# Performance work log

Measured on AMD Instinct MI355X. Metric: run time of the kernel, lower is better.

The kernel has to match this reference:

```python
import jax, jax.numpy as jnp
import numpy as np

N_NODES = 100000
N_EDGES = 600000
F_IN, F_HID, F_OUT = 128, 256, 24
EPS = 0.0  # GINConv default eps=0, train_eps=False


def setup_inputs() -> dict:
    key = jax.random.key(0)
    k1, k2, k3, k4, k5 = jax.random.split(key, 5)
    features = jax.random.normal(k1, (N_NODES, F_IN), dtype=jnp.float32)
    edge_index = jax.random.randint(k2, (2, N_EDGES), 0, N_NODES, dtype=jnp.int64)
    W1 = jax.random.normal(k3, (F_IN, F_HID), dtype=jnp.float32) * (1.0 / np.sqrt(F_IN))
    b1 = jnp.zeros((F_HID,), dtype=jnp.float32)
    W2 = jax.random.normal(k4, (F_HID, F_OUT), dtype=jnp.float32) * (1.0 / np.sqrt(F_HID))
    b2 = jnp.zeros((F_OUT,), dtype=jnp.float32)
    return {"features": features, "edge_index": edge_index,
            "W1": W1, "b1": b1, "W2": W2, "b2": b2}


def gin_conv(x, src, dst, W, b):
    # sum-aggregate neighbor features: agg[i] = sum_{(j->i)} x[j]
    agg = jax.ops.segment_sum(x[src], dst, num_segments=N_NODES)
    h = (1.0 + EPS) * x + agg
    return h @ W + b


def reference(features, edge_index, W1, b1, W2, b2):
    src, dst = edge_index[0], edge_index[1]
    h = gin_conv(features, src, dst, W1, b1)
    h = jax.nn.relu(h)
    # dropout is identity in eval mode (training=False)
    h = gin_conv(h, src, dst, W2, b2)
    return jax.nn.log_softmax(h, axis=1)
```

## Files before the change

### kernel.cpp

```cpp
#include <hip/hip_runtime.h>
#include <hip/hip_bf16.h>
#include <math.h>

#define N_NODES 100000
#define N_EDGES 600000
#define F_IN 128
#define F_HID 256
#define F_OUT 24
#define SCAN_NB 98

typedef __attribute__((ext_vector_type(8))) short bf16x8;
typedef __attribute__((ext_vector_type(4))) float f32x4;

__device__ inline unsigned short f2bf(float f) {
  __hip_bfloat16 h = __float2bfloat16(f);
  return *reinterpret_cast<unsigned short*>(&h);
}
__device__ inline float bf2f(unsigned short u) {
  return __uint_as_float(((unsigned int)u) << 16);
}

__global__ __launch_bounds__(256) void hist_rank(const int* __restrict__ dst,
                                                 int* __restrict__ deg,
                                                 int* __restrict__ rank) {
  int e = blockIdx.x * 256 + threadIdx.x;
  if (e >= N_EDGES) return;
  rank[e] = atomicAdd(&deg[dst[e]], 1);
}

__global__ __launch_bounds__(256) void scan_partial(
    const int* __restrict__ deg, int* __restrict__ blocksum) {
  int t = threadIdx.x;
  int base = blockIdx.x * 1024 + t * 4;
  int s = 0;
  if (base + 3 < N_NODES) {
    int4 v = *(const int4*)(deg + base);
    s = v.x + v.y + v.z + v.w;
  } else {
    for (int i = base; i < N_NODES; ++i) s += deg[i];
  }
  __shared__ int red[4];
#pragma unroll
  for (int off = 32; off >= 1; off >>= 1) s += __shfl_down(s, off, 64);
  if ((t & 63) == 0) red[t >> 6] = s;
  __syncthreads();
  if (t == 0) blocksum[blockIdx.x] = red[0] + red[1] + red[2] + red[3];
}

__global__ __launch_bounds__(128) void scan_blocksums(int* __restrict__ bs) {
  __shared__ int sh[128];
  int t = threadIdx.x;
  int v = (t < SCAN_NB) ? bs[t] : 0;
  sh[t] = v;
  __syncthreads();
  for (int off = 1; off < 128; off <<= 1) {
    int u = (t >= off) ? sh[t - off] : 0;
    __syncthreads();
    sh[t] += u;
    __syncthreads();
  }
  if (t < SCAN_NB) bs[t] = sh[t] - v;
}

__global__ __launch_bounds__(256) void scan_final(
    const int* __restrict__ deg, const int* __restrict__ blocksum,
    int* __restrict__ row_start) {
  __shared__ int sh[256];
  int t = threadIdx.x;
  int base = blockIdx.x * 1024 + t * 4;
  int d[4] = {0, 0, 0, 0};
  if (base + 3 < N_NODES) {
    int4 v = *(const int4*)(deg + base);
    d[0] = v.x; d[1] = v.y; d[2] = v.z; d[3] = v.w;
  } else {
#pragma unroll
    for (int i = 0; i < 4; ++i)
      if (base + i < N_NODES) d[i] = deg[base + i];
  }
  int ts = d[0] + d[1] + d[2] + d[3];
  sh[t] = ts;
  __syncthreads();
  for (int off = 1; off < 256; off <<= 1) {
    int u = (t >= off) ? sh[t - off] : 0;
    __syncthreads();
    sh[t] += u;
    __syncthreads();
  }
  int run = blocksum[blockIdx.x] + sh[t] - ts;
#pragma unroll
  for (int i = 0; i < 4; ++i) {
    if (base + i < N_NODES) row_start[base + i] = run;
    run += d[i];
  }
}

__global__ __launch_bounds__(256) void fill_csr(
    const int* __restrict__ src, const int* __restrict__ dst,
    const int* __restrict__ row_start, const int* __restrict__ rank,
    int* __restrict__ eidx) {
  int e = blockIdx.x * 256 + threadIdx.x;
  if (e >= N_EDGES) return;
  eidx[row_start[dst[e]] + rank[e]] = src[e];
}

__global__ __launch_bounds__(256) void prep_xbf(
    const float* __restrict__ x, unsigned int* __restrict__ xb) {
  const int n8 = N_NODES * F_IN / 8;
  int i = blockIdx.x * 256 + threadIdx.x;
  int stride = gridDim.x * 256;
  for (; i < n8; i += stride) {
    float4 a = ((const float4*)x)[i * 2];
    float4 b = ((const float4*)x)[i * 2 + 1];
    uint4 o;
    o.x = (unsigned)f2bf(a.x) | ((unsigned)f2bf(a.y) << 16);
    o.y = (unsigned)f2bf(a.z) | ((unsigned)f2bf(a.w) << 16);
    o.z = (unsigned)f2bf(b.x) | ((unsigned)f2bf(b.y) << 16);
    o.w = (unsigned)f2bf(b.z) | ((unsigned)f2bf(b.w) << 16);
    ((uint4*)xb)[i] = o;
  }
}

__global__ __launch_bounds__(256) void prep_w1t(
    const float* __restrict__ W1, unsigned short* __restrict__ w1t) {
  int i = blockIdx.x * 256 + threadIdx.x;
  if (i >= F_IN * F_HID) return;
  int n = i >> 7, k = i & 127;
  w1t[i] = f2bf(W1[k * F_HID + n]);
}

__global__ __launch_bounds__(256) void agg1_gather(
    const unsigned short* __restrict__ xb, const int* __restrict__ row_start,
    const int* __restrict__ deg, const int* __restrict__ eidx,
    unsigned short* __restrict__ h_pre) {
  int g = threadIdx.x >> 5;
  int l = threadIdx.x & 31;
  int node = blockIdx.x * 8 + g;
  if (node >= N_NODES) return;
  int col = l * 4;

  ushort4 sv = *(const ushort4*)(xb + (size_t)node * F_IN + col);
  float a0 = bf2f(sv.x), a1 = bf2f(sv.y), a2 = bf2f(sv.z), a3 = bf2f(sv.w);

  int rs = row_start[node];
  int dg = deg[node];
  for (int base = 0; base < dg; base += 32) {
    int cnt = min(32, dg - base);
    int myidx = (l < cnt) ? eidx[rs + base + l] : 0;
    int j = 0;
    for (; j + 4 <= cnt; j += 4) {
      int s0 = __shfl(myidx, j + 0, 32);
      int s1 = __shfl(myidx, j + 1, 32);
      int s2 = __shfl(myidx, j + 2, 32);
      int s3 = __shfl(myidx, j + 3, 32);
      ushort4 v0 = *(const ushort4*)(xb + (size_t)s0 * F_IN + col);
      ushort4 v1 = *(const ushort4*)(xb + (size_t)s1 * F_IN + col);
      ushort4 v2 = *(const ushort4*)(xb + (size_t)s2 * F_IN + col);
      ushort4 v3 = *(const ushort4*)(xb + (size_t)s3 * F_IN + col);
      a0 += bf2f(v0.x) + bf2f(v1.x) + bf2f(v2.x) + bf2f(v3.x);
      a1 += bf2f(v0.y) + bf2f(v1.y) + bf2f(v2.y) + bf2f(v3.y);
      a2 += bf2f(v0.z) + bf2f(v1.z) + bf2f(v2.z) + bf2f(v3.z);
      a3 += bf2f(v0.w) + bf2f(v1.w) + bf2f(v2.w) + bf2f(v3.w);
    }
    for (; j < cnt; ++j) {
      int s = __shfl(myidx, j, 32);
      ushort4 v = *(const ushort4*)(xb + (size_t)s * F_IN + col);
      a0 += bf2f(v.x);
      a1 += bf2f(v.y);
      a2 += bf2f(v.z);
      a3 += bf2f(v.w);
    }
  }
  ushort4 o;
  o.x = f2bf(a0); o.y = f2bf(a1); o.z = f2bf(a2); o.w = f2bf(a3);
  *(ushort4*)(h_pre + (size_t)node * F_IN + col) = o;
}

__global__ __launch_bounds__(256) void gemm1_mfma(
    const unsigned short* __restrict__ hpre,
    const unsigned short* __restrict__ w1t,
    const float* __restrict__ b1, __hip_bfloat16* __restrict__ h1) {
  __shared__ unsigned char smem[64 * 264 * 2];
  int t = threadIdx.x;
  int lane = t & 63;
  int w = t >> 6;
  int m0 = blockIdx.x * 64;

  for (int ci = t; ci < 1024; ci += 256) {
    int r = ci >> 4;
    int c8 = ci & 15;
    int gr = m0 + r;
    uint4 v = make_uint4(0, 0, 0, 0);
    if (gr < N_NODES) v = *(const uint4*)(hpre + (size_t)gr * F_IN + c8 * 8);
    int byte = (r * 256 + c8 * 16) ^ ((r & 7) << 4);
    *(uint4*)(smem + byte) = v;
  }

  int fl = lane & 15;
  int fk = (lane >> 4) * 8;
  bf16x8 bfrag[4][4];
#pragma unroll
  for (int nt = 0; nt < 4; ++nt)
#pragma unroll
    for (int ks = 0; ks < 4; ++ks)
      bfrag[nt][ks] = *(const bf16x8*)(
          w1t + (size_t)(w * 64 + nt * 16 + fl) * F_IN + ks * 32 + fk);

  __syncthreads();

  f32x4 acc[4][4];
#pragma unroll
  for (int mt = 0; mt < 4; ++mt)
#pragma unroll
    for (int nt = 0; nt < 4; ++nt) acc[mt][nt] = f32x4{0.f, 0.f, 0.f, 0.f};

#pragma unroll
  for (int mt = 0; mt < 4; ++mt) {
    bf16x8 afrag[4];
#pragma unroll
    for (int ks = 0; ks < 4; ++ks) {
      int r = mt * 16 + fl;
      int byte = (r * 256 + (ks * 32 + fk) * 2) ^ ((r & 7) << 4);
      afrag[ks] = *(const bf16x8*)(smem + byte);
    }
#pragma unroll
    for (int nt = 0; nt < 4; ++nt)
#pragma unroll
      for (int ks = 0; ks < 4; ++ks)
        acc[mt][nt] = __builtin_amdgcn_mfma_f32_16x16x32_bf16(
            afrag[ks], bfrag[nt][ks], acc[mt][nt], 0, 0, 0);
  }

  __syncthreads();
  unsigned short* Csm = (unsigned short*)smem;
  const int CS = 264;
  int rb = (lane >> 4) * 4;
#pragma unroll
  for (int mt = 0; mt < 4; ++mt) {
#pragma unroll
    for (int nt = 0; nt < 4; ++nt) {
      int gcol = w * 64 + nt * 16 + fl;
      float bias = b1[gcol];
#pragma unroll
      for (int j = 0; j < 4; ++j) {
        float v = fmaxf(acc[mt][nt][j] + bias, 0.f);
        Csm[(mt * 16 + rb + j) * CS + gcol] = f2bf(v);
      }
    }
  }
  __syncthreads();
  for (int ci = t; ci < 2048; ci += 256) {
    int r = ci >> 5, c16 = ci & 31;
    int grow = m0 + r;
    if (grow < N_NODES) {
      uint4 v = *(const uint4*)(Csm + r * CS + c16 * 8);
      *(uint4*)((unsigned short*)h1 + (size_t)grow * F_HID + c16 * 8) = v;
    }
  }
}

__global__ __launch_bounds__(256) void gemm2(
    const __hip_bfloat16* __restrict__ h1, const float* __restrict__ W2,
    float* __restrict__ z0) {
  __shared__ float w2s[F_HID * F_OUT];
  int t = threadIdx.x;
  for (int i = t; i < F_HID * F_OUT; i += 256) w2s[i] = W2[i];
  __syncthreads();
  int row = blockIdx.x * 256 + t;
  if (row >= N_NODES) return;
  const uint4* hp = reinterpret_cast<const uint4*>(h1 + (size_t)row * F_HID);
  float acc[F_OUT];
#pragma unroll
  for (int j = 0; j < F_OUT; ++j) acc[j] = 0.f;

  for (int kc = 0; kc < F_HID / 8; ++kc) {
    uint4 u = hp[kc];
    float a[8];
    a[0] = __uint_as_float(u.x << 16);
    a[1] = __uint_as_float(u.x & 0xffff0000u);
    a[2] = __uint_as_float(u.y << 16);
    a[3] = __uint_as_float(u.y & 0xffff0000u);
    a[4] = __uint_as_float(u.z << 16);
    a[5] = __uint_as_float(u.z & 0xffff0000u);
    a[6] = __uint_as_float(u.w << 16);
    a[7] = __uint_as_float(u.w & 0xffff0000u);
#pragma unroll
    for (int j = 0; j < 8; ++j) {
      int k = kc * 8 + j;
      const float4* w4 = (const float4*)&w2s[k * F_OUT];
      float4 b0 = w4[0], b1v = w4[1], b2v = w4[2];
      float4 b3 = w4[3], b4 = w4[4], b5 = w4[5];
      float av = a[j];
      acc[0] += av * b0.x;  acc[1] += av * b0.y;
      acc[2] += av * b0.z;  acc[3] += av * b0.w;
      acc[4] += av * b1v.x; acc[5] += av * b1v.y;
      acc[6] += av * b1v.z; acc[7] += av * b1v.w;
      acc[8] += av * b2v.x; acc[9] += av * b2v.y;
      acc[10] += av * b2v.z; acc[11] += av * b2v.w;
      acc[12] += av * b3.x; acc[13] += av * b3.y;
      acc[14] += av * b3.z; acc[15] += av * b3.w;
      acc[16] += av * b4.x; acc[17] += av * b4.y;
      acc[18] += av * b4.z; acc[19] += av * b4.w;
      acc[20] += av * b5.x; acc[21] += av * b5.y;
      acc[22] += av * b5.z; acc[23] += av * b5.w;
    }
  }
  float* zp = z0 + (size_t)row * F_OUT;
#pragma unroll
  for (int j = 0; j < F_OUT; ++j) zp[j] = acc[j];
}

__global__ __launch_bounds__(256) void agg2_finalize(
    const float* __restrict__ z0, const int* __restrict__ row_start,
    const int* __restrict__ deg, const int* __restrict__ eidx,
    const float* __restrict__ b2, float* __restrict__ out) {
  int g = threadIdx.x >> 5;
  int c = threadIdx.x & 31;
  int node = blockIdx.x * 8 + g;
  if (node >= N_NODES) return;
  bool act = (c < F_OUT);
  float v = act ? (z0[(size_t)node * F_OUT + c] + b2[c]) : 0.f;

  int rs = row_start[node];
  int dg = deg[node];
  for (int base = 0; base < dg; base += 32) {
    int cnt = min(32, dg - base);
    int myidx = (c < cnt) ? eidx[rs + base + c] : 0;
    int j = 0;
    for (; j + 4 <= cnt; j += 4) {
      int s0 = __shfl(myidx, j + 0, 32);
      int s1 = __shfl(myidx, j + 1, 32);
      int s2 = __shfl(myidx, j + 2, 32);
      int s3 = __shfl(myidx, j + 3, 32);
      float v0 = act ? z0[(size_t)s0 * F_OUT + c] : 0.f;
      float v1 = act ? z0[(size_t)s1 * F_OUT + c] : 0.f;
      float v2 = act ? z0[(size_t)s2 * F_OUT + c] : 0.f;
      float v3 = act ? z0[(size_t)s3 * F_OUT + c] : 0.f;
      v += (v0 + v1) + (v2 + v3);
    }
    for (; j < cnt; ++j) {
      int s = __shfl(myidx, j, 32);
      v += act ? z0[(size_t)s * F_OUT + c] : 0.f;
    }
  }

  float mx = act ? v : -1e30f;
#pragma unroll
  for (int m = 16; m >= 1; m >>= 1) mx = fmaxf(mx, __shfl_xor(mx, m, 32));
  float e = act ? __expf(v - mx) : 0.f;
#pragma unroll
  for (int m = 16; m >= 1; m >>= 1) e += __shfl_xor(e, m, 32);
  float lse = mx + __logf(e);
  if (act) out[(size_t)node * F_OUT + c] = v - lse;
}

extern "C" void kernel_launch(void* const* d_in, const int* in_sizes, int n_in,
                              void* d_out, int out_size, void* d_ws,
                              size_t ws_size, hipStream_t stream) {
  const float* x = (const float*)d_in[0];
  const int* ei = (const int*)d_in[1];
  const float* W1 = (const float*)d_in[2];
  const float* b1 = (const float*)d_in[3];
  const float* W2 = (const float*)d_in[4];
  const float* b2 = (const float*)d_in[5];
  const int* src = ei;
  const int* dst = ei + N_EDGES;

  char* ws = (char*)d_ws;
  int* deg = (int*)ws;
  int* row_start = (int*)(ws + 400000);
  int* rank = (int*)(ws + 800000);
  int* eidx = (int*)(ws + 3200000);
  unsigned short* xb = (unsigned short*)(ws + 5600000);
  unsigned short* h_pre = (unsigned short*)(ws + 31200000);
  __hip_bfloat16* h1 = (__hip_bfloat16*)(ws + 56800000);
  float* z0 = (float*)(ws + 108000000);
  int* blocksum = (int*)(ws + 117600000);
  unsigned short* w1t = (unsigned short*)(ws + 117600400);
  float* out = (float*)d_out;

  hipMemsetAsync(ws, 0, 400000, stream);

  const int EB = (N_EDGES + 255) / 256;
  hist_rank<<<EB, 256, 0, stream>>>(dst, deg, rank);

  scan_partial<<<SCAN_NB, 256, 0, stream>>>(deg, blocksum);
  scan_blocksums<<<1, 128, 0, stream>>>(blocksum);
  scan_final<<<SCAN_NB, 256, 0, stream>>>(deg, blocksum, row_start);

  fill_csr<<<EB, 256, 0, stream>>>(src, dst, row_start, rank, eidx);

  prep_xbf<<<2048, 256, 0, stream>>>(x, (unsigned int*)xb);
  prep_w1t<<<(F_IN * F_HID + 255) / 256, 256, 0, stream>>>(W1, w1t);

  agg1_gather<<<(N_NODES + 7) / 8, 256, 0, stream>>>(xb, row_start, deg,
                                                     eidx, h_pre);

  gemm1_mfma<<<(N_NODES + 63) / 64, 256, 0, stream>>>(h_pre, w1t, b1, h1);

  gemm2<<<(N_NODES + 255) / 256, 256, 0, stream>>>(h1, W2, z0);

  agg2_finalize<<<(N_NODES + 7) / 8, 256, 0, stream>>>(z0, row_start, deg,
                                                       eidx, b2, out);
}
```

Before: 267.0 us.

## Fuse second GEMM into first GEMM epilogue using MFMA on LDS-resident hidden tile

The relu'd hidden tile already sitting in shared memory is now multiplied directly by a bf16, transposed and zero-padded W2 using MFMA instructions, writing only the 24-wide z0 output. This removes the global write and re-read of the 100000x256 bf16 hidden activations, along with the separate scalar FMA gemm2 launch. The weight-prep kernels are merged into one launch that also builds the padded W2 copy. In exchange, W2 is rounded to bf16 and the MFMA tiles pad the 24 output columns to 32.

```diff
diff --git a/kernel.cpp b/kernel.cpp
--- a/kernel.cpp
+++ b/kernel.cpp
@@ -103,12 +103,14 @@
   eidx[row_start[dst[e]] + rank[e]] = src[e];
 }
 
-__global__ __launch_bounds__(256) void prep_xbf(
-    const float* __restrict__ x, unsigned int* __restrict__ xb) {
+__global__ __launch_bounds__(256) void prep_all(
+    const float* __restrict__ x, const float* __restrict__ W1,
+    const float* __restrict__ W2, unsigned int* __restrict__ xb,
+    unsigned short* __restrict__ w1t, unsigned short* __restrict__ w2b) {
   const int n8 = N_NODES * F_IN / 8;
-  int i = blockIdx.x * 256 + threadIdx.x;
+  int tid = blockIdx.x * 256 + threadIdx.x;
   int stride = gridDim.x * 256;
-  for (; i < n8; i += stride) {
+  for (int i = tid; i < n8; i += stride) {
     float4 a = ((const float4*)x)[i * 2];
     float4 b = ((const float4*)x)[i * 2 + 1];
     uint4 o;
@@ -118,14 +120,14 @@
     o.w = (unsigned)f2bf(b.z) | ((unsigned)f2bf(b.w) << 16);
     ((uint4*)xb)[i] = o;
   }
-}
-
-__global__ __launch_bounds__(256) void prep_w1t(
-    const float* __restrict__ W1, unsigned short* __restrict__ w1t) {
-  int i = blockIdx.x * 256 + threadIdx.x;
-  if (i >= F_IN * F_HID) return;
-  int n = i >> 7, k = i & 127;
-  w1t[i] = f2bf(W1[k * F_HID + n]);
+  for (int i = tid; i < F_IN * F_HID; i += stride) {
+    int n = i >> 7, k = i & 127;
+    w1t[i] = f2bf(W1[k * F_HID + n]);
+  }
+  for (int i = tid; i < 32 * F_HID; i += stride) {
+    int c = i >> 8, k = i & 255;
+    w2b[i] = (c < F_OUT) ? f2bf(W2[k * F_OUT + c]) : 0;
+  }
 }
 
 __global__ __launch_bounds__(256) void agg1_gather(
@@ -175,10 +177,11 @@
   *(ushort4*)(h_pre + (size_t)node * F_IN + col) = o;
 }
 
-__global__ __launch_bounds__(256) void gemm1_mfma(
+__global__ __launch_bounds__(256) void gemm12_fused(
     const unsigned short* __restrict__ hpre,
     const unsigned short* __restrict__ w1t,
-    const float* __restrict__ b1, __hip_bfloat16* __restrict__ h1) {
+    const unsigned short* __restrict__ w2b,
+    const float* __restrict__ b1, float* __restrict__ z0) {
   __shared__ unsigned char smem[64 * 264 * 2];
   int t = threadIdx.x;
   int lane = t & 63;
@@ -248,65 +251,36 @@
     }
   }
   __syncthreads();
-  for (int ci = t; ci < 2048; ci += 256) {
-    int r = ci >> 5, c16 = ci & 31;
-    int grow = m0 + r;
-    if (grow < N_NODES) {
-      uint4 v = *(const uint4*)(Csm + r * CS + c16 * 8);
-      *(uint4*)((unsigned short*)h1 + (size_t)grow * F_HID + c16 * 8) = v;
-    }
-  }
-}
-
-__global__ __launch_bounds__(256) void gemm2(
-    const __hip_bfloat16* __restrict__ h1, const float* __restrict__ W2,
-    float* __restrict__ z0) {
-  __shared__ float w2s[F_HID * F_OUT];
-  int t = threadIdx.x;
-  for (int i = t; i < F_HID * F_OUT; i += 256) w2s[i] = W2[i];
-  __syncthreads();
-  int row = blockIdx.x * 256 + t;
-  if (row >= N_NODES) return;
-  const uint4* hp = reinterpret_cast<const uint4*>(h1 + (size_t)row * F_HID);
-  float acc[F_OUT];
-#pragma unroll
-  for (int j = 0; j < F_OUT; ++j) acc[j] = 0.f;
-
-  for (int kc = 0; kc < F_HID / 8; ++kc) {
-    uint4 u = hp[kc];
-    float a[8];
-    a[0] = __uint_as_float(u.x << 16);
-    a[1] = __uint_as_float(u.x & 0xffff0000u);
-    a[2] = __uint_as_float(u.y << 16);
-    a[3] = __uint_as_float(u.y & 0xffff0000u);
-    a[4] = __uint_as_float(u.z << 16);
-    a[5] = __uint_as_float(u.z & 0xffff0000u);
-    a[6] = __uint_as_float(u.w << 16);
-    a[7] = __uint_as_float(u.w & 0xffff0000u);
-#pragma unroll
-    for (int j = 0; j < 8; ++j) {
-      int k = kc * 8 + j;
-      const float4* w4 = (const float4*)&w2s[k * F_OUT];
-      float4 b0 = w4[0], b1v = w4[1], b2v = w4[2];
-      float4 b3 = w4[3], b4 = w4[4], b5 = w4[5];
-      float av = a[j];
-      acc[0] += av * b0.x;  acc[1] += av * b0.y;
-      acc[2] += av * b0.z;  acc[3] += av * b0.w;
-      acc[4] += av * b1v.x; acc[5] += av * b1v.y;
-      acc[6] += av * b1v.z; acc[7] += av * b1v.w;
-      acc[8] += av * b2v.x; acc[9] += av * b2v.y;
-      acc[10] += av * b2v.z; acc[11] += av * b2v.w;
-      acc[12] += av * b3.x; acc[13] += av * b3.y;
-      acc[14] += av * b3.z; acc[15] += av * b3.w;
-      acc[16] += av * b4.x; acc[17] += av * b4.y;
-      acc[18] += av * b4.z; acc[19] += av * b4.w;
-      acc[20] += av * b5.x; acc[21] += av * b5.y;
-      acc[22] += av * b5.z; acc[23] += av * b5.w;
-    }
-  }
-  float* zp = z0 + (size_t)row * F_OUT;
-#pragma unroll
-  for (int j = 0; j < F_OUT; ++j) zp[j] = acc[j];
+
+  bf16x8 b2frag[2][8];
+#pragma unroll
+  for (int ct = 0; ct < 2; ++ct)
+#pragma unroll
+    for (int ks = 0; ks < 8; ++ks)
+      b2frag[ct][ks] = *(const bf16x8*)(
+          w2b + (size_t)(ct * 16 + fl) * F_HID + ks * 32 + fk);
+
+  f32x4 zacc[2] = {f32x4{0.f, 0.f, 0.f, 0.f}, f32x4{0.f, 0.f, 0.f, 0.f}};
+#pragma unroll
+  for (int ks = 0; ks < 8; ++ks) {
+    bf16x8 a2 = *(const bf16x8*)(Csm + (w * 16 + fl) * CS + ks * 32 + fk);
+#pragma unroll
+    for (int ct = 0; ct < 2; ++ct)
+      zacc[ct] = __builtin_amdgcn_mfma_f32_16x16x32_bf16(a2, b2frag[ct][ks],
+                                                         zacc[ct], 0, 0, 0);
+  }
+
+#pragma unroll
+  for (int ct = 0; ct < 2; ++ct) {
+    int gcol = ct * 16 + fl;
+    if (gcol < F_OUT) {
+#pragma unroll
+      for (int j = 0; j < 4; ++j) {
+        int grow = m0 + w * 16 + rb + j;
+        if (grow < N_NODES) z0[(size_t)grow * F_OUT + gcol] = zacc[ct][j];
+      }
+    }
+  }
 }
 
 __global__ __launch_bounds__(256) void agg2_finalize(
@@ -372,10 +346,10 @@
   int* eidx = (int*)(ws + 3200000);
   unsigned short* xb = (unsigned short*)(ws + 5600000);
   unsigned short* h_pre = (unsigned short*)(ws + 31200000);
-  __hip_bfloat16* h1 = (__hip_bfloat16*)(ws + 56800000);
-  float* z0 = (float*)(ws + 108000000);
-  int* blocksum = (int*)(ws + 117600000);
-  unsigned short* w1t = (unsigned short*)(ws + 117600400);
+  float* z0 = (float*)(ws + 56800000);
+  int* blocksum = (int*)(ws + 66400000);
+  unsigned short* w1t = (unsigned short*)(ws + 66400400);
+  unsigned short* w2b = (unsigned short*)(ws + 66465936);
   float* out = (float*)d_out;
 
   hipMemsetAsync(ws, 0, 400000, stream);
@@ -389,15 +363,13 @@
 
   fill_csr<<<EB, 256, 0, stream>>>(src, dst, row_start, rank, eidx);
 
-  prep_xbf<<<2048, 256, 0, stream>>>(x, (unsigned int*)xb);
-  prep_w1t<<<(F_IN * F_HID + 255) / 256, 256, 0, stream>>>(W1, w1t);
+  prep_all<<<2048, 256, 0, stream>>>(x, W1, W2, (unsigned int*)xb, w1t, w2b);
 
   agg1_gather<<<(N_NODES + 7) / 8, 256, 0, stream>>>(xb, row_start, deg,
                                                      eidx, h_pre);
 
-  gemm1_mfma<<<(N_NODES + 63) / 64, 256, 0, stream>>>(h_pre, w1t, b1, h1);
-
-  gemm2<<<(N_NODES + 255) / 256, 256, 0, stream>>>(h1, W2, z0);
+  gemm12_fused<<<(N_NODES + 63) / 64, 256, 0, stream>>>(h_pre, w1t, w2b, b1,
+                                                        z0);
 
   agg2_finalize<<<(N_NODES + 7) / 8, 256, 0, stream>>>(z0, row_start, deg,
                                                        eidx, b2, out);
```

Result: faster. 238.4 us (-10.7%).
